# Performance work log

Hardware: AMD Instinct MI355X
Metric: run time of the kernel (lower is better)

## Reference

```python
import jax, jax.numpy as jnp
import numpy as np

B, S, E, H, N = 16384, 256, 128, 128, 34  # batch, state_dim, reduced_lang_dim, mlp hidden, N_task
TEMP = 0.1
EPS = 1e-8  # torch cosine_similarity eps


def setup_inputs() -> dict:
    key = jax.random.key(0)
    ks = jax.random.split(key, 12)
    sc = 0.05
    return {
        "state": jax.random.normal(ks[0], (B, S), dtype=jnp.float32),
        "task_id": jax.random.randint(ks[1], (B,), 0, N),
        "prior": jax.random.normal(ks[2], (B, N), dtype=jnp.float32),
        # stacked weights of the 34 per-task MLPs (Linear(S,H) -> ReLU -> Linear(H,H) -> ReLU -> Linear(H,E))
        "W1": jax.random.normal(ks[3], (N, S, H), dtype=jnp.float32) * sc,
        "b1": jax.random.normal(ks[4], (N, H), dtype=jnp.float32) * sc,
        "W2": jax.random.normal(ks[5], (N, H, H), dtype=jnp.float32) * sc,
        "b2": jax.random.normal(ks[6], (N, H), dtype=jnp.float32) * sc,
        "W3": jax.random.normal(ks[7], (N, H, E), dtype=jnp.float32) * sc,
        "b3": jax.random.normal(ks[8], (N, E), dtype=jnp.float32) * sc,
        "lang_emb": jax.random.normal(ks[9], (N, E), dtype=jnp.float32),
    }


def reference(state, task_id, prior, W1, b1, W2, b2, W3, b3, lang_emb):
    # 34 parallel MLPs as a single batched GEMM stack: [B,S] x [N,S,H] -> [B,N,H]
    h = jax.nn.relu(jnp.einsum('bs,nsh->bnh', state, W1) + b1)
    h = jax.nn.relu(jnp.einsum('bnh,nhk->bnk', h, W2) + b2)
    q = jnp.einsum('bnk,nke->bne', h, W3) + b3            # [B,N,E]
    # normalize (torch.norm division, no eps, then cosine_similarity renormalizes -> unit)
    q = q / jnp.linalg.norm(q, axis=-1, keepdims=True)
    lang = lang_emb[task_id]                              # [B,E]
    lang_n = lang / jnp.maximum(jnp.linalg.norm(lang, axis=-1, keepdims=True), EPS)
    cos_sim = jnp.einsum('bne,be->bn', q, lang_n)         # [B,N]
    log_task_prob = jax.nn.log_softmax(cos_sim / TEMP, axis=-1)
    task_prob_prior = jax.nn.softmax(prior, axis=-1)      # exp(log_softmax(prior))
    latent_vec = jnp.einsum('bne,bn->be', q, task_prob_prior)
    latent_target = jax.lax.stop_gradient(q[jnp.arange(B), task_id])  # detach
    rep_vec = jnp.concatenate([state, latent_vec], axis=-1)           # [B, S+E]
    return rep_vec, log_task_prob, latent_target, latent_vec
```

## Files before the change

### kernel.cpp

```cpp
#include <hip/hip_runtime.h>
#include <hip/hip_bf16.h>
#include <hip/hip_fp16.h>
#include <cstdint>
#include <cstddef>

typedef __bf16 bf16;
typedef __attribute__((ext_vector_type(8))) __bf16 bf16x8;
typedef __attribute__((ext_vector_type(16))) float f32x16;

static_assert(sizeof(bf16x8) == 16, "bf16x8 must be 16B");

#define NTASK 34
#define BTOT 16384
#define WSTRIDE 73728

__device__ __forceinline__ f32x16 mfma32(bf16x8 a, bf16x8 b, f32x16 c) {
  return __builtin_amdgcn_mfma_f32_32x32x16_bf16(a, b, c, 0, 0, 0);
}

__device__ __forceinline__ void gload_lds16(const void* g, void* l) {
  __builtin_amdgcn_global_load_lds((__attribute__((address_space(1))) void*)g,
                                   (__attribute__((address_space(3))) void*)l,
                                   16, 0, 0);
}

__device__ __forceinline__ unsigned pack2(float lo, float hi) {
  union { __bf16 h[2]; unsigned u; } v;
  v.h[0] = (__bf16)lo; v.h[1] = (__bf16)hi;
  return v.u;
}

__device__ __forceinline__ void pl32swap(unsigned &a, unsigned &b) {
  asm volatile("v_permlane32_swap_b32 %0, %1" : "+v"(a), "+v"(b));
}

__global__ void prep_all(const float* __restrict__ W1, const float* __restrict__ W2,
                         const float* __restrict__ W3, const float* __restrict__ b1,
                         const float* __restrict__ b2, const float* __restrict__ b3,
                         const float* __restrict__ state, const float* __restrict__ prior,
                         bf16* __restrict__ wdst, bf16* __restrict__ sdst,
                         float* __restrict__ ppt) {
  int bid = blockIdx.x;
  if (bid < 1224) {
    int idx = bid * 256 + threadIdx.x;
    int n = idx / 9216;
    int r = idx - n * 9216;
    int g = r >> 8;
    int m = (r >> 6) & 3;
    int l = r & 63;
    int col = m * 32 + (l & 31);
    int kj = (l >> 5) << 3;
    bf16x8 v;
#pragma unroll
    for (int j = 0; j < 8; ++j) v[j] = (bf16)0.f;
    if (g < 16) {
      const float* s = W1 + ((size_t)n * 256 + g * 16 + kj) * 128 + col;
#pragma unroll
      for (int j = 0; j < 8; ++j) v[j] = (bf16)s[(size_t)j * 128];
    } else if (g == 16) {
      if (l < 32) v[0] = (bf16)b1[n * 128 + col];
    } else if (g == 17) {
    } else if (g < 26) {
      const float* s = W2 + ((size_t)n * 128 + (g - 18) * 16 + kj) * 128 + col;
#pragma unroll
      for (int j = 0; j < 8; ++j) v[j] = (bf16)s[(size_t)j * 128];
    } else if (g == 26) {
      if (l < 32) v[0] = (bf16)b2[n * 128 + col];
    } else if (g < 35) {
      const float* s = W3 + ((size_t)n * 128 + (g - 27) * 16 + kj) * 128 + col;
#pragma unroll
      for (int j = 0; j < 8; ++j) v[j] = (bf16)s[(size_t)j * 128];
    } else {
      if (l < 32) v[0] = (bf16)b3[n * 128 + col];
    }
    *(bf16x8*)(wdst + (size_t)n * WSTRIDE + (size_t)(g * 4 + m) * 512 + l * 8) = v;
  } else if (bid < 3272) {
    int idx = (bid - 1224) * 256 + threadIdx.x;
    int rb = idx >> 10;
    int r = idx & 1023;
    int ks = r >> 6;
    int l = r & 63;
    int b = rb * 32 + (l & 31);
    int k0 = ks * 16 + ((l >> 5) << 3);
    const float* s = state + (size_t)b * 256 + k0;
    bf16x8 v;
#pragma unroll
    for (int j = 0; j < 8; ++j) v[j] = (bf16)s[j];
    *(bf16x8*)(sdst + (size_t)(rb * 16 + ks) * 512 + l * 8) = v;
  } else {
    int row = (bid - 3272) * 4 + (threadIdx.x >> 6);
    int lane = threadIdx.x & 63;
    float v = (lane < NTASK) ? prior[(size_t)row * NTASK + lane] : -INFINITY;
    float m = v;
#pragma unroll
    for (int mm = 1; mm < 64; mm <<= 1) m = fmaxf(m, __shfl_xor(m, mm));
    float e = (lane < NTASK) ? expf(v - m) : 0.0f;
    float s = e;
#pragma unroll
    for (int mm = 1; mm < 64; mm <<= 1) s += __shfl_xor(s, mm);
    if (lane < NTASK) ppt[(size_t)lane * BTOT + row] = e / s;
  }
}

__global__ void prep_langn(const float* __restrict__ lang, float* __restrict__ out) {
  __shared__ float red[2];
  int n = blockIdx.x;
  int t = threadIdx.x;
  float v = lang[(size_t)n * 128 + t];
  float ss = v * v;
#pragma unroll
  for (int m = 1; m < 64; m <<= 1) ss += __shfl_xor(ss, m);
  if ((t & 63) == 0) red[t >> 6] = ss;
  __syncthreads();
  float s = red[0] + red[1];
  float sc = 1.0f / fmaxf(sqrtf(s), 1e-8f);
  out[(size_t)n * 128 + t] = v * sc;
}


__global__ void __launch_bounds__(256, 2)
pass1_kernel(const int* __restrict__ task_id, const bf16* __restrict__ wstream,
             const bf16* __restrict__ sf, const float* __restrict__ langn,
             const float* __restrict__ pp_t,
             float* __restrict__ cs_t, __half* __restrict__ lat_part,
             float* __restrict__ out_tgt) {
  __shared__ __align__(16) bf16 shW[3 * 12288];

  const int tid = threadIdx.x;
  const int l = tid & 63;
  const int wid = tid >> 6;
  const int hi = l >> 5;
  const int b = l & 31;
  const int tg = blockIdx.x >> 7;
  const int rg = blockIdx.x & 127;
  const int start = (tg < 2) ? tg * 9 : (18 + (tg - 2) * 8);
  const int cnt = (tg < 2) ? 9 : 8;
  const int nwin = cnt * 6;
  const int row0 = rg * 128 + wid * 32 + b;
  const int rb0 = rg * 4 + wid;

  const int tidn = task_id[row0];
  const bf16* sb = sf + (size_t)rb0 * 8192 + l * 8;
  const bf16* wsrc = wstream + (size_t)start * WSTRIDE;

#define STAGE_WIN(slot, w) \
  { _Pragma("unroll") \
    for (int c = 0; c < 6; ++c) \
      gload_lds16(wsrc + (size_t)(w) * 12288 + c * 2048 + tid * 8, \
                  shW + (slot) * 12288 + c * 2048 + tid * 8); }

#define WIN_TOP() \
  { asm volatile("s_waitcnt vmcnt(6)" ::: "memory"); \
    __builtin_amdgcn_s_barrier(); }

#define KMFMA(slot, gi, bop) \
  { _Pragma("unroll") \
    for (int mt = 0; mt < 4; ++mt) { \
      bf16x8 wf = *(const bf16x8*)(shW + (slot) * 12288 + ((gi) * 4 + mt) * 512 + l * 8); \
      acc[mt] = mfma32(wf, (bop), acc[mt]); } }

  STAGE_WIN(0, 0);
  STAGE_WIN(1, 1);
  bf16x8 sring[16];
#pragma unroll
  for (int i = 0; i < 16; ++i) sring[i] = *(const bf16x8*)(sb + i * 512);

  union { unsigned u[4]; bf16x8 v; } cf;
  cf.u[0] = (l < 32) ? 0x3f80u : 0u;
  cf.u[1] = 0u; cf.u[2] = 0u; cf.u[3] = 0u;

  f32x16 z;
#pragma unroll
  for (int i = 0; i < 16; ++i) z[i] = 0.f;
  f32x16 lat[4] = {z, z, z, z};

  auto transition = [&](f32x16* acc, bf16x8* f) {
#pragma unroll
    for (int mt = 0; mt < 4; ++mt) {
      unsigned p[8];
#pragma unroll
      for (int q = 0; q < 4; ++q) {
        p[2 * q]     = pack2(fmaxf(acc[mt][4 * q + 0], 0.f), fmaxf(acc[mt][4 * q + 1], 0.f));
        p[2 * q + 1] = pack2(fmaxf(acc[mt][4 * q + 2], 0.f), fmaxf(acc[mt][4 * q + 3], 0.f));
      }
      pl32swap(p[0], p[2]); pl32swap(p[1], p[3]);
      pl32swap(p[4], p[6]); pl32swap(p[5], p[7]);
      union { unsigned u[4]; bf16x8 v; } e, o;
      e.u[0] = p[0]; e.u[1] = p[1]; e.u[2] = p[2]; e.u[3] = p[3];
      o.u[0] = p[4]; o.u[1] = p[5]; o.u[2] = p[6]; o.u[3] = p[7];
      f[2 * mt] = e.v; f[2 * mt + 1] = o.v;
    }
  };

  for (int t = 0; t < cnt; ++t) {
    const int n = start + t;
    const int w0g = t * 6;
    f32x16 acc[4];
    bf16x8 f2[8], f3[8];

    WIN_TOP();
    if (w0g + 2 < nwin) STAGE_WIN((w0g + 2) % 3, w0g + 2);
#pragma unroll
    for (int mt = 0; mt < 4; ++mt) acc[mt] = z;
    __builtin_amdgcn_s_setprio(1);
#pragma unroll
    for (int gi = 0; gi < 6; ++gi) KMFMA((w0g) % 3, gi, sring[gi]);
    __builtin_amdgcn_s_setprio(0);

    WIN_TOP();
    if (w0g + 3 < nwin) STAGE_WIN((w0g + 3) % 3, w0g + 3);
    __builtin_amdgcn_s_setprio(1);
#pragma unroll
    for (int gi = 0; gi < 6; ++gi) KMFMA((w0g + 1) % 3, gi, sring[6 + gi]);
    __builtin_amdgcn_s_setprio(0);

    WIN_TOP();
    if (w0g + 4 < nwin) STAGE_WIN((w0g + 4) % 3, w0g + 4);
    __builtin_amdgcn_s_setprio(1);
#pragma unroll
    for (int gi = 0; gi < 4; ++gi) KMFMA((w0g + 2) % 3, gi, sring[12 + gi]);
    KMFMA((w0g + 2) % 3, 4, cf.v);
    __builtin_amdgcn_s_setprio(0);
    transition(acc, f2);

    WIN_TOP();
    if (w0g + 5 < nwin) STAGE_WIN((w0g + 5) % 3, w0g + 5);
#pragma unroll
    for (int mt = 0; mt < 4; ++mt) acc[mt] = z;
    __builtin_amdgcn_s_setprio(1);
#pragma unroll
    for (int gi = 0; gi < 6; ++gi) KMFMA((w0g + 3) % 3, gi, f2[gi]);
    __builtin_amdgcn_s_setprio(0);

    WIN_TOP();
    if (w0g + 6 < nwin) STAGE_WIN((w0g + 6) % 3, w0g + 6);
    __builtin_amdgcn_s_setprio(1);
    KMFMA((w0g + 4) % 3, 0, f2[6]);
    KMFMA((w0g + 4) % 3, 1, f2[7]);
    KMFMA((w0g + 4) % 3, 2, cf.v);
    __builtin_amdgcn_s_setprio(0);
    transition(acc, f3);
#pragma unroll
    for (int mt = 0; mt < 4; ++mt) acc[mt] = z;
    __builtin_amdgcn_s_setprio(1);
    KMFMA((w0g + 4) % 3, 3, f3[0]);
    KMFMA((w0g + 4) % 3, 4, f3[1]);
    KMFMA((w0g + 4) % 3, 5, f3[2]);
    __builtin_amdgcn_s_setprio(0);

    WIN_TOP();
    if (w0g + 7 < nwin) STAGE_WIN((w0g + 7) % 3, w0g + 7);
    __builtin_amdgcn_s_setprio(1);
#pragma unroll
    for (int gi = 0; gi < 5; ++gi) KMFMA((w0g + 5) % 3, gi, f3[3 + gi]);
    KMFMA((w0g + 5) % 3, 5, cf.v);
    __builtin_amdgcn_s_setprio(0);

    float ssq = 0.f, dot = 0.f;
    const float* lgb = langn + (size_t)tidn * 128;
#pragma unroll
    for (int mt = 0; mt < 4; ++mt)
#pragma unroll
      for (int q = 0; q < 4; ++q) {
        int c0 = mt * 32 + q * 8 + 4 * hi;
        float4 lg = *(const float4*)(lgb + c0);
        float a0 = acc[mt][4 * q + 0], a1 = acc[mt][4 * q + 1];
        float a2 = acc[mt][4 * q + 2], a3 = acc[mt][4 * q + 3];
        ssq += a0 * a0 + a1 * a1 + a2 * a2 + a3 * a3;
        dot += a0 * lg.x + a1 * lg.y + a2 * lg.z + a3 * lg.w;
      }
    ssq += __shfl_xor(ssq, 32);
    dot += __shfl_xor(dot, 32);
    float inv = rsqrtf(ssq);
    if (l < 32) cs_t[(size_t)row0 * NTASK + n] = dot * inv;
    float pwi = pp_t[(size_t)n * BTOT + row0] * inv;
#pragma unroll
    for (int mt = 0; mt < 4; ++mt) lat[mt] += acc[mt] * pwi;
    if (tidn == n) {
#pragma unroll
      for (int mt = 0; mt < 4; ++mt)
#pragma unroll
        for (int q = 0; q < 4; ++q) {
          float4 qv = {acc[mt][4 * q + 0] * inv, acc[mt][4 * q + 1] * inv,
                       acc[mt][4 * q + 2] * inv, acc[mt][4 * q + 3] * inv};
          *(float4*)(out_tgt + (size_t)row0 * 128 + mt * 32 + q * 8 + 4 * hi) = qv;
        }
    }
  }

  __half* lp = lat_part + ((size_t)tg * BTOT + row0) * 128;
#pragma unroll
  for (int mt = 0; mt < 4; ++mt)
#pragma unroll
    for (int q = 0; q < 4; ++q) {
      int c0 = mt * 32 + q * 8 + 4 * hi;
      union { __half h[4]; uint2 u; } v;
      v.h[0] = __float2half(lat[mt][4 * q + 0]);
      v.h[1] = __float2half(lat[mt][4 * q + 1]);
      v.h[2] = __float2half(lat[mt][4 * q + 2]);
      v.h[3] = __float2half(lat[mt][4 * q + 3]);
      *(uint2*)(lp + c0) = v.u;
    }
#undef STAGE_WIN
#undef WIN_TOP
#undef KMFMA
}


__global__ void __launch_bounds__(256)
pass3_kernel(const float* __restrict__ state, const float* __restrict__ cs_t,
             const __half* __restrict__ lat_part,
             float* __restrict__ out_rep, float* __restrict__ out_ltp,
             float* __restrict__ out_lat) {
  int w = threadIdx.x >> 6, l = threadIdx.x & 63;
  size_t row = (size_t)blockIdx.x * 4 + w;

  float c = (l < NTASK) ? cs_t[row * NTASK + l] * 10.0f : -1e30f;
  float cm = c;
#pragma unroll
  for (int mm = 1; mm < 64; mm <<= 1) cm = fmaxf(cm, __shfl_xor(cm, mm));
  float ce = (l < NTASK) ? expf(c - cm) : 0.0f;
  float cs = ce;
#pragma unroll
  for (int mm = 1; mm < 64; mm <<= 1) cs += __shfl_xor(cs, mm);
  if (l < NTASK) out_ltp[row * NTASK + l] = c - cm - logf(cs);

  float2 lv = {0.f, 0.f};
#pragma unroll
  for (int g = 0; g < 4; ++g) {
    __half2 p = *(const __half2*)(lat_part + ((size_t)g * BTOT + row) * 128 + 2 * l);
    lv.x += __low2float(p);
    lv.y += __high2float(p);
  }
  *(float2*)(out_lat + row * 128 + 2 * l) = lv;
  *(float2*)(out_rep + row * 384 + 256 + 2 * l) = lv;

  float4 sv = *(const float4*)(state + row * 256 + l * 4);
  *(float4*)(out_rep + row * 384 + l * 4) = sv;
}


extern "C" void kernel_launch(void* const* d_in, const int* in_sizes, int n_in,
                              void* d_out, int out_size, void* d_ws, size_t ws_size,
                              hipStream_t stream) {
  (void)in_sizes; (void)n_in; (void)out_size; (void)ws_size;
  const float* state = (const float*)d_in[0];
  const int* task_id = (const int*)d_in[1];
  const float* prior = (const float*)d_in[2];
  const float* W1 = (const float*)d_in[3];
  const float* b1 = (const float*)d_in[4];
  const float* W2 = (const float*)d_in[5];
  const float* b2 = (const float*)d_in[6];
  const float* W3 = (const float*)d_in[7];
  const float* b3 = (const float*)d_in[8];
  const float* lang = (const float*)d_in[9];

  char* ws = (char*)d_ws;
  bf16* wstream  = (bf16*)(ws + 0);
  bf16* sf       = (bf16*)(ws + 5013504);
  float* langn   = (float*)(ws + 13402112);
  float* pp_t    = (float*)(ws + 13419520);
  float* cs_t    = (float*)(ws + 15647744);
  __half* lat_part = (__half*)(ws + 17875968);

  float* out = (float*)d_out;
  float* out_rep = out;
  float* out_ltp = out + 6291456;
  float* out_tgt = out + 6848512;
  float* out_lat = out + 8945664;

  prep_all<<<7368, 256, 0, stream>>>(W1, W2, W3, b1, b2, b3, state, prior,
                                     wstream, sf, pp_t);
  prep_langn<<<NTASK, 128, 0, stream>>>(lang, langn);
  pass1_kernel<<<512, 256, 0, stream>>>(task_id, wstream, sf, langn, pp_t,
                                        cs_t, lat_part, out_tgt);
  pass3_kernel<<<4096, 256, 0, stream>>>(state, cs_t, lat_part,
                                         out_rep, out_ltp, out_lat);
}
```

Baseline: 133.8 us.

## Fuse lang normalization into prep and epilogue into pass1 via last-block counter

The separate lang-embedding normalization kernel becomes 34 extra blocks of prep_all. The pass3 epilogue (log-softmax, latent partial reduction, state copy into rep) moves into pass1: the task-group-0 blocks copy state, and the last of the four task-group blocks for each row group, detected with an atomic counter, finishes the row group. This removes two kernel launches and their gaps, at the cost of a memset, threadfences and a serialized tail that runs in only 128 blocks.

Result: slower. 252.3 us (+88.5%).

```diff
diff --git a/kernel.cpp b/kernel.cpp
--- a/kernel.cpp
+++ b/kernel.cpp
@@ -38,8 +38,10 @@
                          const float* __restrict__ W3, const float* __restrict__ b1,
                          const float* __restrict__ b2, const float* __restrict__ b3,
                          const float* __restrict__ state, const float* __restrict__ prior,
+                         const float* __restrict__ lang,
                          bf16* __restrict__ wdst, bf16* __restrict__ sdst,
-                         float* __restrict__ ppt) {
+                         float* __restrict__ ppt, float* __restrict__ langn) {
+  __shared__ float red[2];
   int bid = blockIdx.x;
   if (bid < 1224) {
     int idx = bid * 256 + threadIdx.x;
@@ -87,7 +89,7 @@
 #pragma unroll
     for (int j = 0; j < 8; ++j) v[j] = (bf16)s[j];
     *(bf16x8*)(sdst + (size_t)(rb * 16 + ks) * 512 + l * 8) = v;
-  } else {
+  } else if (bid < 7368) {
     int row = (bid - 3272) * 4 + (threadIdx.x >> 6);
     int lane = threadIdx.x & 63;
     float v = (lane < NTASK) ? prior[(size_t)row * NTASK + lane] : -INFINITY;
@@ -99,32 +101,37 @@
 #pragma unroll
     for (int mm = 1; mm < 64; mm <<= 1) s += __shfl_xor(s, mm);
     if (lane < NTASK) ppt[(size_t)lane * BTOT + row] = e / s;
+  } else {
+    int n = bid - 7368;
+    int t = threadIdx.x;
+    float v = 0.f, ss = 0.f;
+    if (t < 128) {
+      v = lang[(size_t)n * 128 + t];
+      ss = v * v;
+#pragma unroll
+      for (int m = 1; m < 64; m <<= 1) ss += __shfl_xor(ss, m);
+      if ((t & 63) == 0) red[t >> 6] = ss;
+    }
+    __syncthreads();
+    if (t < 128) {
+      float s = red[0] + red[1];
+      float sc = 1.0f / fmaxf(sqrtf(s), 1e-8f);
+      langn[(size_t)n * 128 + t] = v * sc;
+    }
   }
-}
-
-__global__ void prep_langn(const float* __restrict__ lang, float* __restrict__ out) {
-  __shared__ float red[2];
-  int n = blockIdx.x;
-  int t = threadIdx.x;
-  float v = lang[(size_t)n * 128 + t];
-  float ss = v * v;
-#pragma unroll
-  for (int m = 1; m < 64; m <<= 1) ss += __shfl_xor(ss, m);
-  if ((t & 63) == 0) red[t >> 6] = ss;
-  __syncthreads();
-  float s = red[0] + red[1];
-  float sc = 1.0f / fmaxf(sqrtf(s), 1e-8f);
-  out[(size_t)n * 128 + t] = v * sc;
 }
 
 
 __global__ void __launch_bounds__(256, 2)
 pass1_kernel(const int* __restrict__ task_id, const bf16* __restrict__ wstream,
              const bf16* __restrict__ sf, const float* __restrict__ langn,
-             const float* __restrict__ pp_t,
+             const float* __restrict__ pp_t, const float* __restrict__ state,
              float* __restrict__ cs_t, __half* __restrict__ lat_part,
-             float* __restrict__ out_tgt) {
+             int* __restrict__ counter,
+             float* __restrict__ out_rep, float* __restrict__ out_ltp,
+             float* __restrict__ out_tgt, float* __restrict__ out_lat) {
   __shared__ __align__(16) bf16 shW[3 * 12288];
+  __shared__ int lastflag;
 
   const int tid = threadIdx.x;
   const int l = tid & 63;
@@ -301,42 +308,49 @@
       v.h[3] = __float2half(lat[mt][4 * q + 3]);
       *(uint2*)(lp + c0) = v.u;
     }
+
+  if (tg == 0) {
+#pragma unroll 4
+    for (int it = 0; it < 32; ++it) {
+      int r = (rg << 7) + it * 4 + (tid >> 6);
+      float4 v = *(const float4*)(state + (size_t)r * 256 + (tid & 63) * 4);
+      *(float4*)(out_rep + (size_t)r * 384 + (tid & 63) * 4) = v;
+    }
+  }
+
+  __threadfence();
+  __syncthreads();
+  if (tid == 0) lastflag = (atomicAdd(&counter[rg], 1) == 3);
+  __syncthreads();
+  if (!lastflag) return;
+  __threadfence();
+
+  for (int it = 0; it < 32; ++it) {
+    int ll = tid & 63;
+    size_t row = ((size_t)rg << 7) + it * 4 + (tid >> 6);
+    float c = (ll < NTASK) ? cs_t[row * NTASK + ll] * 10.0f : -1e30f;
+    float cm = c;
+#pragma unroll
+    for (int mm = 1; mm < 64; mm <<= 1) cm = fmaxf(cm, __shfl_xor(cm, mm));
+    float ce = (ll < NTASK) ? expf(c - cm) : 0.0f;
+    float cssum = ce;
+#pragma unroll
+    for (int mm = 1; mm < 64; mm <<= 1) cssum += __shfl_xor(cssum, mm);
+    if (ll < NTASK) out_ltp[row * NTASK + ll] = c - cm - logf(cssum);
+
+    float2 lv = {0.f, 0.f};
+#pragma unroll
+    for (int g = 0; g < 4; ++g) {
+      __half2 p = *(const __half2*)(lat_part + ((size_t)g * BTOT + row) * 128 + 2 * ll);
+      lv.x += __low2float(p);
+      lv.y += __high2float(p);
+    }
+    *(float2*)(out_lat + row * 128 + 2 * ll) = lv;
+    *(float2*)(out_rep + row * 384 + 256 + 2 * ll) = lv;
+  }
 #undef STAGE_WIN
 #undef WIN_TOP
 #undef KMFMA
-}
-
-
-__global__ void __launch_bounds__(256)
-pass3_kernel(const float* __restrict__ state, const float* __restrict__ cs_t,
-             const __half* __restrict__ lat_part,
-             float* __restrict__ out_rep, float* __restrict__ out_ltp,
-             float* __restrict__ out_lat) {
-  int w = threadIdx.x >> 6, l = threadIdx.x & 63;
-  size_t row = (size_t)blockIdx.x * 4 + w;
-
-  float c = (l < NTASK) ? cs_t[row * NTASK + l] * 10.0f : -1e30f;
-  float cm = c;
-#pragma unroll
-  for (int mm = 1; mm < 64; mm <<= 1) cm = fmaxf(cm, __shfl_xor(cm, mm));
-  float ce = (l < NTASK) ? expf(c - cm) : 0.0f;
-  float cs = ce;
-#pragma unroll
-  for (int mm = 1; mm < 64; mm <<= 1) cs += __shfl_xor(cs, mm);
-  if (l < NTASK) out_ltp[row * NTASK + l] = c - cm - logf(cs);
-
-  float2 lv = {0.f, 0.f};
-#pragma unroll
-  for (int g = 0; g < 4; ++g) {
-    __half2 p = *(const __half2*)(lat_part + ((size_t)g * BTOT + row) * 128 + 2 * l);
-    lv.x += __low2float(p);
-    lv.y += __high2float(p);
-  }
-  *(float2*)(out_lat + row * 128 + 2 * l) = lv;
-  *(float2*)(out_rep + row * 384 + 256 + 2 * l) = lv;
-
-  float4 sv = *(const float4*)(state + row * 256 + l * 4);
-  *(float4*)(out_rep + row * 384 + l * 4) = sv;
 }
 
 
@@ -362,6 +376,7 @@
   float* pp_t    = (float*)(ws + 13419520);
   float* cs_t    = (float*)(ws + 15647744);
   __half* lat_part = (__half*)(ws + 17875968);
+  int* counter   = (int*)(ws + 34653184);
 
   float* out = (float*)d_out;
   float* out_rep = out;
@@ -369,11 +384,10 @@
   float* out_tgt = out + 6848512;
   float* out_lat = out + 8945664;
 
-  prep_all<<<7368, 256, 0, stream>>>(W1, W2, W3, b1, b2, b3, state, prior,
-                                     wstream, sf, pp_t);
-  prep_langn<<<NTASK, 128, 0, stream>>>(lang, langn);
-  pass1_kernel<<<512, 256, 0, stream>>>(task_id, wstream, sf, langn, pp_t,
-                                        cs_t, lat_part, out_tgt);
-  pass3_kernel<<<4096, 256, 0, stream>>>(state, cs_t, lat_part,
-                                         out_rep, out_ltp, out_lat);
-}
+  hipMemsetAsync(counter, 0, 512, stream);
+  prep_all<<<7402, 256, 0, stream>>>(W1, W2, W3, b1, b2, b3, state, prior, lang,
+                                     wstream, sf, pp_t, langn);
+  pass1_kernel<<<512, 256, 0, stream>>>(task_id, wstream, sf, langn, pp_t, state,
+                                        cs_t, lat_part, counter,
+                                        out_rep, out_ltp, out_tgt, out_lat);
+}
```
